# Optimization experiments

Measured on AMD Instinct MI355X. Metric: run time of the kernel, lower is better.

The kernel has to match this reference:

```python
import jax, jax.numpy as jnp
import numpy as np

EMBED_DIM = 768
HEADS = 8
HEAD_DIM = 128  # gnn_hidden_dim
OUT_DIM = HEADS * HEAD_DIM  # 1024, concat=True
NEG_SLOPE = 0.2  # PyG GATConv leaky_relu slope


def setup_inputs() -> dict:
    key = jax.random.key(0)
    ks = jax.random.split(key, 12)
    N, E = 10000, 160000
    x = jax.random.normal(ks[0], (N, EMBED_DIM), dtype=jnp.float32)
    edge_index = jax.random.randint(ks[1], (2, E), 0, N, dtype=jnp.int32)
    edge_attr = jax.random.uniform(ks[2], (E, 1), dtype=jnp.float32)
    # GATConv params (single layer, edge_dim=1)
    sc = 1.0 / np.sqrt(EMBED_DIM)
    W = jax.random.normal(ks[3], (EMBED_DIM, OUT_DIM), dtype=jnp.float32) * sc
    att_src = jax.random.normal(ks[4], (HEADS, HEAD_DIM), dtype=jnp.float32) * 0.1
    att_dst = jax.random.normal(ks[5], (HEADS, HEAD_DIM), dtype=jnp.float32) * 0.1
    W_edge = jax.random.normal(ks[6], (1, OUT_DIM), dtype=jnp.float32)
    att_edge = jax.random.normal(ks[7], (HEADS, HEAD_DIM), dtype=jnp.float32) * 0.1
    bias = jnp.zeros((OUT_DIM,), dtype=jnp.float32)
    # final classifier: in = 3*OUT_DIM (global pool + text node + image node)
    clf_W = jax.random.normal(ks[8], (3 * OUT_DIM, 2), dtype=jnp.float32) * (1.0 / np.sqrt(3 * OUT_DIM))
    clf_b = jnp.zeros((2,), dtype=jnp.float32)
    return {
        'x': x, 'edge_index': edge_index, 'edge_attr': edge_attr,
        'text_idx': 0, 'image_idx': 1,
        'W': W, 'att_src': att_src, 'att_dst': att_dst,
        'W_edge': W_edge, 'att_edge': att_edge, 'bias': bias,
        'clf_W': clf_W, 'clf_b': clf_b,
    }


def gat_layer(x, edge_index, edge_attr, W, att_src, att_dst, W_edge, att_edge, bias):
    N = x.shape[0]
    # add self-loops with edge_attr = mean of existing edge_attr (PyG default fill_value='mean')
    loop = jnp.arange(N, dtype=edge_index.dtype)
    ei = jnp.concatenate([edge_index, jnp.stack([loop, loop])], axis=1)
    ea_mean = jnp.mean(edge_attr, axis=0, keepdims=True)
    ea = jnp.concatenate([edge_attr, jnp.broadcast_to(ea_mean, (N, edge_attr.shape[1]))], axis=0)
    src, dst = ei[0], ei[1]
    xs = (x @ W).reshape(N, HEADS, HEAD_DIM)             # [N, H, C]
    a_src = jnp.einsum('nhc,hc->nh', xs, att_src)        # per-node src logits
    a_dst = jnp.einsum('nhc,hc->nh', xs, att_dst)
    e_emb = (ea @ W_edge).reshape(-1, HEADS, HEAD_DIM)   # [Etot, H, C]
    a_edge = jnp.einsum('ehc,hc->eh', e_emb, att_edge)
    alpha = jax.nn.leaky_relu(a_src[src] + a_dst[dst] + a_edge, NEG_SLOPE)  # [Etot, H]
    # softmax over incoming edges of each dst node
    m = jax.ops.segment_max(alpha, dst, num_segments=N)
    ex = jnp.exp(alpha - m[dst])
    denom = jax.ops.segment_sum(ex, dst, num_segments=N)
    w = ex / denom[dst]                                  # normalized attention [Etot, H]
    msg = xs[src] * w[:, :, None]                        # [Etot, H, C]
    out = jax.ops.segment_sum(msg, dst, num_segments=N)  # [N, H, C]
    return out.reshape(N, OUT_DIM) + bias


def reference(x, edge_index, edge_attr, text_idx, image_idx,
              W, att_src, att_dst, W_edge, att_edge, bias, clf_W, clf_b):
    # single GAT layer (num_gat_layers=1 -> no ELU/dropout after, eval mode)
    h = gat_layer(x, edge_index, edge_attr, W, att_src, att_dst, W_edge, att_edge, bias)
    g = jnp.mean(h, axis=0, keepdims=True)               # global_mean_pool, batch=None
    t = h[text_idx][None, :]
    im = h[image_idx][None, :]
    fused = jnp.concatenate([g, t, im], axis=1)          # [1, 3*OUT_DIM]
    logits = fused @ clf_W + clf_b                       # [1, 2]
    return logits
```

## Files before the change

### kernel.cpp

```cpp
#include <hip/hip_runtime.h>

#define NN 10000
#define EE 160000
#define ETOT (EE + NN)
#define EMB 768
#define ODIM 1024
#define NEG 0.2f
#define CAP 56

#define OFF_PT     0
#define OFF_Q      12288
#define OFF_EAACC  12296
#define OFF_CNTD   12304
#define OFF_CNTS   22304
#define ZERO_START 12296
#define ZERO_CNT   20008
#define OFF_A      32304
#define OFF_EDD    192304
#define OFF_EDS    1312304
#define OFF_EX     2432304
#define OFF_RDEN   3792304
#define OFF_S      3872304
#define OFF_Z      3952304
#define OFF_YPART  3964592

__global__ __launch_bounds__(256) void k1f(
    const float* __restrict__ W, const float* __restrict__ att_src,
    const float* __restrict__ att_dst, const float* __restrict__ W_edge,
    const float* __restrict__ att_edge, const float* __restrict__ edge_attr,
    const int* __restrict__ ei, const float* __restrict__ bias,
    const float* __restrict__ clf_W, const float* __restrict__ clf_b,
    float* __restrict__ out, float* __restrict__ ws) {
  __shared__ float red[8];
  int b = blockIdx.x;
  int* wsI = (int*)ws;
  if (b < 48) {
    int tid = b * 256 + threadIdx.x;
    int k = tid >> 4, j = tid & 15, h = j & 7;
    const float* att = (j < 8) ? att_src : att_dst;
    const float* wp = W + k * ODIM + h * 128;
    const float* ap = att + h * 128;
    float acc = 0.f;
    #pragma unroll 8
    for (int c = 0; c < 128; ++c) acc += wp[c] * ap[c];
    ws[OFF_PT + j * 768 + k] = acc;
  } else if (b == 48) {
    if (threadIdx.x < 8) {
      int h = threadIdx.x;
      float acc = 0.f;
      #pragma unroll 8
      for (int c = 0; c < 128; ++c) acc += W_edge[h * 128 + c] * att_edge[h * 128 + c];
      ws[OFF_Q + h] = acc;
    }
  } else if (b < 113) {
    int bi = b - 49;
    float acc = 0.f;
    for (int i = bi * 256 + threadIdx.x; i < EE; i += 64 * 256) acc += edge_attr[i];
    #pragma unroll
    for (int off = 32; off > 0; off >>= 1) acc += __shfl_down(acc, off, 64);
    if ((threadIdx.x & 63) == 0) atomicAdd(&ws[OFF_EAACC], acc);
  } else if (b < 778) {
    int e = (b - 113) * 256 + threadIdx.x;
    if (e >= ETOT) return;
    int src, dst;
    if (e < EE) { src = ei[e]; dst = ei[EE + e]; } else { src = dst = e - EE; }
    int pd = atomicAdd(&wsI[OFF_CNTD + dst], 1);
    if (pd < CAP) ((int2*)(wsI + OFF_EDD))[dst * CAP + pd] = make_int2(e, src);
    int ps = atomicAdd(&wsI[OFF_CNTS + src], 1);
    if (ps < CAP) ((int2*)(wsI + OFF_EDS))[src * CAP + ps] = make_int2(e, dst);
  } else {
    int t = threadIdx.x;
    float b0 = 0.f, b1 = 0.f;
    for (int i = t; i < 3072; i += 256) {
      float f = bias[i & 1023];
      b0 += f * clf_W[2 * i];
      b1 += f * clf_W[2 * i + 1];
    }
    #pragma unroll
    for (int o = 32; o > 0; o >>= 1) {
      b0 += __shfl_down(b0, o, 64);
      b1 += __shfl_down(b1, o, 64);
    }
    if ((t & 63) == 0) { red[(t >> 6) * 2] = b0; red[(t >> 6) * 2 + 1] = b1; }
    __syncthreads();
    if (t == 0) {
      out[0] = clf_b[0] + red[0] + red[2] + red[4] + red[6];
      out[1] = clf_b[1] + red[1] + red[3] + red[5] + red[7];
    }
  }
}

__global__ __launch_bounds__(256) void kAx(const float* __restrict__ x,
                                           float* __restrict__ ws) {
  __shared__ float sm[12288];
  for (int i = threadIdx.x; i < 3072; i += 256)
    ((float4*)sm)[i] = ((const float4*)(ws + OFF_PT))[i];
  __syncthreads();
  int li = threadIdx.x & 15, nl = threadIdx.x >> 4;
  int n = blockIdx.x * 16 + nl;
  float a[16];
  #pragma unroll
  for (int j = 0; j < 16; ++j) a[j] = 0.f;
  const float4* xr = (const float4*)(x + n * EMB);
  const float4* pT4 = (const float4*)sm;
  for (int i = 0; i < 12; ++i) {
    float4 xv = xr[li + i * 16];
    int k4 = li + i * 16;
    #pragma unroll
    for (int j = 0; j < 16; ++j) {
      float4 p = pT4[j * 192 + k4];
      a[j] += xv.x * p.x + xv.y * p.y + xv.z * p.z + xv.w * p.w;
    }
  }
  __syncthreads();
  #pragma unroll
  for (int j = 0; j < 16; ++j) sm[threadIdx.x * 17 + j] = a[j];
  __syncthreads();
  int rn = threadIdx.x >> 4, rj = threadIdx.x & 15;
  float s = 0.f;
  #pragma unroll
  for (int c = 0; c < 16; ++c) s += sm[(rn * 16 + c) * 17 + rj];
  ws[OFF_A + (blockIdx.x * 16 + rn) * 16 + rj] = s;
}

__global__ __launch_bounds__(256) void kE(const int* __restrict__ ei,
                                          const float* __restrict__ edge_attr,
                                          float* __restrict__ ws) {
  int e = blockIdx.x * 256 + threadIdx.x;
  if (e >= ETOT) return;
  int src, dst; float ea;
  if (e < EE) { src = ei[e]; dst = ei[EE + e]; ea = edge_attr[e]; }
  else { src = dst = e - EE; ea = ws[OFF_EAACC] * (1.0f / EE); }
  const float4* as4 = (const float4*)(ws + OFF_A + src * 16);
  const float4* ad4 = (const float4*)(ws + OFF_A + dst * 16 + 8);
  float4 s0 = as4[0], s1 = as4[1], d0 = ad4[0], d1 = ad4[1];
  float asr[8] = {s0.x, s0.y, s0.z, s0.w, s1.x, s1.y, s1.z, s1.w};
  float ads[8] = {d0.x, d0.y, d0.z, d0.w, d1.x, d1.y, d1.z, d1.w};
  float ex[8];
  #pragma unroll
  for (int h = 0; h < 8; ++h) {
    float v = asr[h] + ads[h] + ea * ws[OFF_Q + h];
    v = (v >= 0.f) ? v : NEG * v;
    ex[h] = __expf(v);
  }
  float4* p = (float4*)(ws + OFF_EX + e * 8);
  p[0] = make_float4(ex[0], ex[1], ex[2], ex[3]);
  p[1] = make_float4(ex[4], ex[5], ex[6], ex[7]);
}

__global__ __launch_bounds__(128) void kD(float* __restrict__ ws) {
  int t = blockIdx.x * 128 + threadIdx.x;
  int dst = t >> 3, h = t & 7;
  const int* wsI = (const int*)ws;
  int deg = wsI[OFF_CNTD + dst]; if (deg > CAP) deg = CAP;
  const int2* edd = (const int2*)(wsI + OFF_EDD) + dst * CAP;
  float den = 0.f;
  for (int j = 0; j < deg; ++j) den += ws[OFF_EX + edd[j].x * 8 + h];
  ws[OFF_RDEN + t] = 1.0f / den;
}

__global__ __launch_bounds__(128) void kSZ(const float* __restrict__ x,
                                           const int* __restrict__ tptr,
                                           const int* __restrict__ iptr,
                                           float* __restrict__ ws) {
  __shared__ float sm[512];
  const int* wsI = (const int*)ws;
  if (blockIdx.x < 625) {
    int t = blockIdx.x * 128 + threadIdx.x;
    int src = t >> 3, h = t & 7;
    int deg = wsI[OFF_CNTS + src]; if (deg > CAP) deg = CAP;
    const int2* eds = (const int2*)(wsI + OFF_EDS) + src * CAP;
    float s = 0.f;
    for (int j = 0; j < deg; ++j) {
      int2 ed = eds[j];
      s += ws[OFF_EX + ed.x * 8 + h] * ws[OFF_RDEN + ed.y * 8 + h];
    }
    ws[OFF_S + t] = s;
  } else {
    float* wL = sm;
    int* srcS = (int*)(sm + 448);
    int* degP = (int*)(sm + 508);
    int r = blockIdx.x - 625;
    int d = r / 6, kc = r % 6;
    int target = (d == 0) ? tptr[0] : iptr[0];
    if (threadIdx.x == 0) {
      int dg = wsI[OFF_CNTD + target];
      degP[0] = (dg > CAP) ? CAP : dg;
    }
    __syncthreads();
    int deg = degP[0];
    for (int idx = threadIdx.x; idx < deg * 8; idx += 128) {
      int j = idx >> 3, h = idx & 7;
      int2 ed = ((const int2*)(wsI + OFF_EDD))[target * CAP + j];
      wL[idx] = ws[OFF_EX + ed.x * 8 + h] * ws[OFF_RDEN + target * 8 + h];
      if (h == 0) srcS[j] = ed.y;
    }
    __syncthreads();
    int col = kc * 128 + threadIdx.x;
    float acc[8];
    #pragma unroll
    for (int h = 0; h < 8; ++h) acc[h] = 0.f;
    for (int j = 0; j < deg; ++j) {
      float xv = x[srcS[j] * EMB + col];
      const float* wv = &wL[j * 8];
      #pragma unroll
      for (int h = 0; h < 8; ++h) acc[h] += wv[h] * xv;
    }
    #pragma unroll
    for (int h = 0; h < 8; ++h) ws[OFF_Z + (d * 8 + h) * EMB + col] = acc[h];
  }
}

__global__ __launch_bounds__(256) void k7s(const float* __restrict__ x,
                                           float* __restrict__ ws) {
  __shared__ float sL[64 * 8];
  int base = blockIdx.x * 64;
  int c = blockIdx.y;
  for (int i = threadIdx.x; i < 512; i += 256) {
    int n = base + (i >> 3);
    sL[i] = (n < NN) ? ws[OFF_S + base * 8 + i] : 0.f;
  }
  __syncthreads();
  int col = c * 256 + threadIdx.x;
  float acc[8];
  #pragma unroll
  for (int h = 0; h < 8; ++h) acc[h] = 0.f;
  int nmax = (NN - base < 64) ? (NN - base) : 64;
  for (int i = 0; i < nmax; ++i) {
    float xv = x[(base + i) * EMB + col];
    const float* sv = &sL[i * 8];
    #pragma unroll
    for (int h = 0; h < 8; ++h) acc[h] += xv * sv[h];
  }
  float* yp = ws + OFF_YPART + blockIdx.x * 6144 + col;
  #pragma unroll
  for (int h = 0; h < 8; ++h) yp[h * 768] = acc[h];
}

__global__ __launch_bounds__(128) void k8(const float* __restrict__ W,
                                          const float* __restrict__ clf_W,
                                          float* __restrict__ out,
                                          float* __restrict__ ws) {
  __shared__ float vL[144];
  __shared__ float red[4];
  int h = blockIdx.x, kc = blockIdx.y, kbase = kc * 48;
  for (int i = threadIdx.x; i < 144; i += 128) {
    int d = i / 48, k = i - d * 48;
    float v;
    if (d == 0) {
      float acc = 0.f;
      for (int b = 0; b < 157; ++b)
        acc += ws[OFF_YPART + b * 6144 + h * 768 + kbase + k];
      v = acc * (1.0f / NN);
    } else {
      v = ws[OFF_Z + ((d - 1) * 8 + h) * 768 + kbase + k];
    }
    vL[i] = v;
  }
  __syncthreads();
  int c = threadIdx.x;
  float a0 = 0.f, a1 = 0.f, a2 = 0.f;
  #pragma unroll 4
  for (int k = 0; k < 48; ++k) {
    float wv = W[(kbase + k) * ODIM + h * 128 + c];
    a0 += vL[k] * wv;
    a1 += vL[48 + k] * wv;
    a2 += vL[96 + k] * wv;
  }
  int ib = h * 128 + c;
  float l0 = a0 * clf_W[2 * ib] + a1 * clf_W[2 * (1024 + ib)]
           + a2 * clf_W[2 * (2048 + ib)];
  float l1 = a0 * clf_W[2 * ib + 1] + a1 * clf_W[2 * (1024 + ib) + 1]
           + a2 * clf_W[2 * (2048 + ib) + 1];
  #pragma unroll
  for (int o = 32; o > 0; o >>= 1) {
    l0 += __shfl_down(l0, o, 64);
    l1 += __shfl_down(l1, o, 64);
  }
  if ((threadIdx.x & 63) == 0) {
    red[(threadIdx.x >> 6) * 2] = l0;
    red[(threadIdx.x >> 6) * 2 + 1] = l1;
  }
  __syncthreads();
  if (threadIdx.x == 0) {
    atomicAdd(&out[0], red[0] + red[2]);
    atomicAdd(&out[1], red[1] + red[3]);
  }
}

extern "C" void kernel_launch(void* const* d_in, const int* in_sizes, int n_in,
                              void* d_out, int out_size, void* d_ws, size_t ws_size,
                              hipStream_t stream) {
  const float* x        = (const float*)d_in[0];
  const int*   ei       = (const int*)d_in[1];
  const float* edge_attr= (const float*)d_in[2];
  const int*   tptr     = (const int*)d_in[3];
  const int*   iptr     = (const int*)d_in[4];
  const float* W        = (const float*)d_in[5];
  const float* att_src  = (const float*)d_in[6];
  const float* att_dst  = (const float*)d_in[7];
  const float* W_edge   = (const float*)d_in[8];
  const float* att_edge = (const float*)d_in[9];
  const float* bias     = (const float*)d_in[10];
  const float* clf_W    = (const float*)d_in[11];
  const float* clf_b    = (const float*)d_in[12];
  float* ws  = (float*)d_ws;
  float* out = (float*)d_out;

  hipMemsetAsync(ws + ZERO_START, 0, ZERO_CNT * sizeof(float), stream);
  k1f<<<779, 256, 0, stream>>>(W, att_src, att_dst, W_edge, att_edge, edge_attr,
                               ei, bias, clf_W, clf_b, out, ws);
  kAx<<<625, 256, 0, stream>>>(x, ws);
  kE<<<665, 256, 0, stream>>>(ei, edge_attr, ws);
  kD<<<625, 128, 0, stream>>>(ws);
  kSZ<<<637, 128, 0, stream>>>(x, tptr, iptr, ws);
  dim3 g7(157, 3);
  k7s<<<g7, 256, 0, stream>>>(x, ws);
  dim3 g8(8, 16);
  k8<<<g8, 128, 0, stream>>>(W, clf_W, out, ws);
}
```

Before: 195.2 us.

## Recompute edge exponentials on the fly and fuse per-source sums with x reduction

Drops the per-edge exp kernel and its ex buffer. The denominator kernel and the per-source kernel now recompute leaky_relu/exp from the node logits and edge_attr. The per-source score computation is fused with the x-weighted partial reduction into one kernel over 32-node tiles, which removes the S buffer and one launch. k8 then reduces twice as many partials with a split accumulation. This trades extra exp arithmetic and gathers for fewer launches and less workspace traffic.

```diff
diff --git a/kernel.cpp b/kernel.cpp
--- a/kernel.cpp
+++ b/kernel.cpp
@@ -18,11 +18,9 @@
 #define OFF_A      32304
 #define OFF_EDD    192304
 #define OFF_EDS    1312304
-#define OFF_EX     2432304
-#define OFF_RDEN   3792304
-#define OFF_S      3872304
-#define OFF_Z      3952304
-#define OFF_YPART  3964592
+#define OFF_RDEN   2432304
+#define OFF_Z      2512304
+#define OFF_YPART  2524592
 
 __global__ __launch_bounds__(256) void k1f(
     const float* __restrict__ W, const float* __restrict__ att_src,
@@ -123,80 +121,101 @@
   ws[OFF_A + (blockIdx.x * 16 + rn) * 16 + rj] = s;
 }
 
-__global__ __launch_bounds__(256) void kE(const int* __restrict__ ei,
-                                          const float* __restrict__ edge_attr,
-                                          float* __restrict__ ws) {
-  int e = blockIdx.x * 256 + threadIdx.x;
-  if (e >= ETOT) return;
-  int src, dst; float ea;
-  if (e < EE) { src = ei[e]; dst = ei[EE + e]; ea = edge_attr[e]; }
-  else { src = dst = e - EE; ea = ws[OFF_EAACC] * (1.0f / EE); }
-  const float4* as4 = (const float4*)(ws + OFF_A + src * 16);
-  const float4* ad4 = (const float4*)(ws + OFF_A + dst * 16 + 8);
-  float4 s0 = as4[0], s1 = as4[1], d0 = ad4[0], d1 = ad4[1];
-  float asr[8] = {s0.x, s0.y, s0.z, s0.w, s1.x, s1.y, s1.z, s1.w};
-  float ads[8] = {d0.x, d0.y, d0.z, d0.w, d1.x, d1.y, d1.z, d1.w};
-  float ex[8];
-  #pragma unroll
-  for (int h = 0; h < 8; ++h) {
-    float v = asr[h] + ads[h] + ea * ws[OFF_Q + h];
-    v = (v >= 0.f) ? v : NEG * v;
-    ex[h] = __expf(v);
-  }
-  float4* p = (float4*)(ws + OFF_EX + e * 8);
-  p[0] = make_float4(ex[0], ex[1], ex[2], ex[3]);
-  p[1] = make_float4(ex[4], ex[5], ex[6], ex[7]);
-}
-
-__global__ __launch_bounds__(128) void kD(float* __restrict__ ws) {
+__global__ __launch_bounds__(128) void kD2(const float* __restrict__ edge_attr,
+                                           float* __restrict__ ws) {
   int t = blockIdx.x * 128 + threadIdx.x;
   int dst = t >> 3, h = t & 7;
   const int* wsI = (const int*)ws;
   int deg = wsI[OFF_CNTD + dst]; if (deg > CAP) deg = CAP;
   const int2* edd = (const int2*)(wsI + OFF_EDD) + dst * CAP;
+  float q = ws[OFF_Q + h];
+  float adst = ws[OFF_A + dst * 16 + 8 + h];
+  float eamean = ws[OFF_EAACC] * (1.0f / EE);
   float den = 0.f;
-  for (int j = 0; j < deg; ++j) den += ws[OFF_EX + edd[j].x * 8 + h];
+  for (int j = 0; j < deg; ++j) {
+    int2 ed = edd[j];
+    float ea = (ed.x < EE) ? edge_attr[ed.x] : eamean;
+    float v = ws[OFF_A + ed.y * 16 + h] + adst + ea * q;
+    v = (v >= 0.f) ? v : NEG * v;
+    den += __expf(v);
+  }
   ws[OFF_RDEN + t] = 1.0f / den;
 }
 
-__global__ __launch_bounds__(128) void kSZ(const float* __restrict__ x,
-                                           const int* __restrict__ tptr,
-                                           const int* __restrict__ iptr,
-                                           float* __restrict__ ws) {
+__global__ __launch_bounds__(256) void k7sz(const float* __restrict__ x,
+                                            const int* __restrict__ ei,
+                                            const float* __restrict__ edge_attr,
+                                            const int* __restrict__ tptr,
+                                            const int* __restrict__ iptr,
+                                            float* __restrict__ ws) {
   __shared__ float sm[512];
   const int* wsI = (const int*)ws;
-  if (blockIdx.x < 625) {
-    int t = blockIdx.x * 128 + threadIdx.x;
-    int src = t >> 3, h = t & 7;
-    int deg = wsI[OFF_CNTS + src]; if (deg > CAP) deg = CAP;
-    const int2* eds = (const int2*)(wsI + OFF_EDS) + src * CAP;
+  const int t = threadIdx.x;
+  if (blockIdx.x < 313) {
+    int base = blockIdx.x * 32;
+    int nl = t >> 3, h = t & 7;
+    int n = base + nl;
     float s = 0.f;
-    for (int j = 0; j < deg; ++j) {
-      int2 ed = eds[j];
-      s += ws[OFF_EX + ed.x * 8 + h] * ws[OFF_RDEN + ed.y * 8 + h];
-    }
-    ws[OFF_S + t] = s;
+    if (n < NN) {
+      int deg = wsI[OFF_CNTS + n]; if (deg > CAP) deg = CAP;
+      const int2* eds = (const int2*)(wsI + OFF_EDS) + n * CAP;
+      float q = ws[OFF_Q + h];
+      float asrc = ws[OFF_A + n * 16 + h];
+      float eamean = ws[OFF_EAACC] * (1.0f / EE);
+      for (int j = 0; j < deg; ++j) {
+        int2 ed = eds[j];
+        float ea = (ed.x < EE) ? edge_attr[ed.x] : eamean;
+        float v = asrc + ws[OFF_A + ed.y * 16 + 8 + h] + ea * q;
+        v = (v >= 0.f) ? v : NEG * v;
+        s += __expf(v) * ws[OFF_RDEN + ed.y * 8 + h];
+      }
+    }
+    sm[t] = s;
+    __syncthreads();
+    float acc[3][8];
+    #pragma unroll
+    for (int c = 0; c < 3; ++c)
+      #pragma unroll
+      for (int h2 = 0; h2 < 8; ++h2) acc[c][h2] = 0.f;
+    int nmax = NN - base; if (nmax > 32) nmax = 32;
+    for (int i = 0; i < nmax; ++i) {
+      const float* xr = x + (base + i) * EMB;
+      float x0 = xr[t], x1 = xr[t + 256], x2 = xr[t + 512];
+      const float* sv = &sm[i * 8];
+      #pragma unroll
+      for (int h2 = 0; h2 < 8; ++h2) {
+        acc[0][h2] += x0 * sv[h2];
+        acc[1][h2] += x1 * sv[h2];
+        acc[2][h2] += x2 * sv[h2];
+      }
+    }
+    float* yp = ws + OFF_YPART + blockIdx.x * 6144;
+    #pragma unroll
+    for (int h2 = 0; h2 < 8; ++h2) {
+      yp[h2 * 768 + t] = acc[0][h2];
+      yp[h2 * 768 + 256 + t] = acc[1][h2];
+      yp[h2 * 768 + 512 + t] = acc[2][h2];
+    }
   } else {
     float* wL = sm;
     int* srcS = (int*)(sm + 448);
-    int* degP = (int*)(sm + 508);
-    int r = blockIdx.x - 625;
-    int d = r / 6, kc = r % 6;
+    int r = blockIdx.x - 313;
+    int d = r / 3, kc = r % 3;
     int target = (d == 0) ? tptr[0] : iptr[0];
-    if (threadIdx.x == 0) {
-      int dg = wsI[OFF_CNTD + target];
-      degP[0] = (dg > CAP) ? CAP : dg;
-    }
-    __syncthreads();
-    int deg = degP[0];
-    for (int idx = threadIdx.x; idx < deg * 8; idx += 128) {
+    int deg = wsI[OFF_CNTD + target]; if (deg > CAP) deg = CAP;
+    float eamean = ws[OFF_EAACC] * (1.0f / EE);
+    for (int idx = t; idx < deg * 8; idx += 256) {
       int j = idx >> 3, h = idx & 7;
       int2 ed = ((const int2*)(wsI + OFF_EDD))[target * CAP + j];
-      wL[idx] = ws[OFF_EX + ed.x * 8 + h] * ws[OFF_RDEN + target * 8 + h];
+      float ea = (ed.x < EE) ? edge_attr[ed.x] : eamean;
+      float v = ws[OFF_A + ed.y * 16 + h] + ws[OFF_A + target * 16 + 8 + h]
+              + ea * ws[OFF_Q + h];
+      v = (v >= 0.f) ? v : NEG * v;
+      wL[idx] = __expf(v) * ws[OFF_RDEN + target * 8 + h];
       if (h == 0) srcS[j] = ed.y;
     }
     __syncthreads();
-    int col = kc * 128 + threadIdx.x;
+    int col = kc * 256 + t;
     float acc[8];
     #pragma unroll
     for (int h = 0; h < 8; ++h) acc[h] = 0.f;
@@ -211,51 +230,31 @@
   }
 }
 
-__global__ __launch_bounds__(256) void k7s(const float* __restrict__ x,
-                                           float* __restrict__ ws) {
-  __shared__ float sL[64 * 8];
-  int base = blockIdx.x * 64;
-  int c = blockIdx.y;
-  for (int i = threadIdx.x; i < 512; i += 256) {
-    int n = base + (i >> 3);
-    sL[i] = (n < NN) ? ws[OFF_S + base * 8 + i] : 0.f;
-  }
-  __syncthreads();
-  int col = c * 256 + threadIdx.x;
-  float acc[8];
-  #pragma unroll
-  for (int h = 0; h < 8; ++h) acc[h] = 0.f;
-  int nmax = (NN - base < 64) ? (NN - base) : 64;
-  for (int i = 0; i < nmax; ++i) {
-    float xv = x[(base + i) * EMB + col];
-    const float* sv = &sL[i * 8];
-    #pragma unroll
-    for (int h = 0; h < 8; ++h) acc[h] += xv * sv[h];
-  }
-  float* yp = ws + OFF_YPART + blockIdx.x * 6144 + col;
-  #pragma unroll
-  for (int h = 0; h < 8; ++h) yp[h * 768] = acc[h];
-}
-
 __global__ __launch_bounds__(128) void k8(const float* __restrict__ W,
                                           const float* __restrict__ clf_W,
                                           float* __restrict__ out,
                                           float* __restrict__ ws) {
+  __shared__ float yred[384];
   __shared__ float vL[144];
   __shared__ float red[4];
   int h = blockIdx.x, kc = blockIdx.y, kbase = kc * 48;
-  for (int i = threadIdx.x; i < 144; i += 128) {
+  for (int i = threadIdx.x; i < 384; i += 128) {
+    int k = i % 48, g = i / 48;
+    float a = 0.f;
+    for (int b = g; b < 313; b += 8)
+      a += ws[OFF_YPART + b * 6144 + h * 768 + kbase + k];
+    yred[i] = a;
+  }
+  for (int i = threadIdx.x; i < 96; i += 128) {
     int d = i / 48, k = i - d * 48;
-    float v;
-    if (d == 0) {
-      float acc = 0.f;
-      for (int b = 0; b < 157; ++b)
-        acc += ws[OFF_YPART + b * 6144 + h * 768 + kbase + k];
-      v = acc * (1.0f / NN);
-    } else {
-      v = ws[OFF_Z + ((d - 1) * 8 + h) * 768 + kbase + k];
-    }
-    vL[i] = v;
+    vL[48 + i] = ws[OFF_Z + (d * 8 + h) * EMB + kbase + k];
+  }
+  __syncthreads();
+  if (threadIdx.x < 48) {
+    float a = 0.f;
+    #pragma unroll
+    for (int g = 0; g < 8; ++g) a += yred[g * 48 + threadIdx.x];
+    vL[threadIdx.x] = a * (1.0f / NN);
   }
   __syncthreads();
   int c = threadIdx.x;
@@ -311,11 +310,8 @@
   k1f<<<779, 256, 0, stream>>>(W, att_src, att_dst, W_edge, att_edge, edge_attr,
                                ei, bias, clf_W, clf_b, out, ws);
   kAx<<<625, 256, 0, stream>>>(x, ws);
-  kE<<<665, 256, 0, stream>>>(ei, edge_attr, ws);
-  kD<<<625, 128, 0, stream>>>(ws);
-  kSZ<<<637, 128, 0, stream>>>(x, tptr, iptr, ws);
-  dim3 g7(157, 3);
-  k7s<<<g7, 256, 0, stream>>>(x, ws);
+  kD2<<<625, 128, 0, stream>>>(edge_attr, ws);
+  k7sz<<<319, 256, 0, stream>>>(x, ei, edge_attr, tptr, iptr, ws);
   dim3 g8(8, 16);
   k8<<<g8, 128, 0, stream>>>(W, clf_W, out, ws);
 }
```

Result: slower. 209.1 us (+7.1%).
